# Optimization experiments

Measured on AMD Instinct MI355X. Metric: run time of the kernel, lower is better.

The kernel has to match this reference:

```python
import jax, jax.numpy as jnp
import numpy as np

N = 16384   # total gate nodes (64 graphs x 256 gates)
B = 64      # graphs in batch
E = 49152   # directed edges (avg in-degree 3)
Q = 32      # qubit_num
F = 256     # feat_dim
D = 2 * F   # node feature dim = 512
H = 2       # heads
A = 128     # action_num


def _gatv2(x, wl, wr, att, b, src, dst, n):
    # PyG GATv2Conv (concat=True, share_weights=False, negative_slope=0.2)
    h, c = att.shape
    xl = (x @ wl).reshape(n, h, c)   # source-side projection [N,H,C]
    xr = (x @ wr).reshape(n, h, c)   # target-side projection [N,H,C]
    e = jax.nn.leaky_relu(xl[src] + xr[dst], 0.2)       # [E,H,C]
    logit = jnp.einsum('ehc,hc->eh', e, att)             # [E,H]
    m = jax.ops.segment_max(logit, dst, num_segments=n)  # softmax over in-edges per target
    p = jnp.exp(logit - m[dst])
    den = jax.ops.segment_sum(p, dst, num_segments=n)
    alpha = p / den[dst]                                 # [E,H]
    out = jax.ops.segment_sum(alpha[:, :, None] * xl[src], dst, num_segments=n)
    return out.reshape(n, h * c) + b


def _forward(x, xt_w1, xt_b1, xt_w2, xt_b2,
             g0_wl, g0_wr, g0_att, g0_b,
             g1_wl, g1_wr, g1_att, g1_b,
             g2_wl, g2_wr, g2_att, g2_b,
             g3_wl, g3_wr, g3_att, g3_b,
             g4_wl, g4_wr, g4_att, g4_b,
             ln_w, ln_b, aggr_t,
             m_w1, m_b1, m_w2, m_b2, m_w3, m_b3,
             edge_index, batch):
    lr = lambda v: jax.nn.leaky_relu(v, 0.01)
    # x_trans: Linear -> LeakyReLU -> Linear, then fold qubit-pairs into one node
    h0 = lr(x @ xt_w1 + xt_b1) @ xt_w2 + xt_b2           # [2N, F]
    cx = h0.reshape(-1, D)                               # [N, 2F]
    n = cx.shape[0]
    # GATv2Conv default add_self_loops=True (inputs contain no self loops)
    sl = jnp.arange(n, dtype=edge_index.dtype)
    src = jnp.concatenate([edge_index[0], sl])
    dst = jnp.concatenate([edge_index[1], sl])
    res = cx
    h = lr(_gatv2(cx, g0_wl, g0_wr, g0_att, g0_b, src, dst, n))
    for wl_, wr_, att_, b_ in ((g1_wl, g1_wr, g1_att, g1_b),
                               (g2_wl, g2_wr, g2_att, g2_b),
                               (g3_wl, g3_wr, g3_att, g3_b)):
        h = lr(_gatv2(h, wl_, wr_, att_, b_, src, dst, n))
    h = lr(_gatv2(h, g4_wl, g4_wr, g4_att, g4_b, src, dst, n))
    h = h + res                                           # residual [N, 2F]
    # PyG LayerNorm(mode='graph'): normalize over nodes AND channels per graph
    cnt = jax.ops.segment_sum(jnp.ones((n,), h.dtype), batch, num_segments=B)
    norm = cnt * h.shape[1]
    mean = jax.ops.segment_sum(h.sum(-1), batch, num_segments=B) / norm
    hc = h - mean[batch][:, None]
    var = jax.ops.segment_sum((hc * hc).sum(-1), batch, num_segments=B) / norm
    h = hc / jnp.sqrt(var + 1e-5)[batch][:, None] * ln_w + ln_b
    # SoftmaxAggregation(learn=True): channel-wise softmax over nodes per graph
    logit = h * aggr_t
    mg = jax.ops.segment_max(logit, batch, num_segments=B)
    p = jnp.exp(logit - mg[batch])
    den = jax.ops.segment_sum(p, batch, num_segments=B)
    g = jax.ops.segment_sum((p / den[batch]) * h, batch, num_segments=B)  # [B, 2F]
    # head MLP 512->384->256->128
    o = lr(g @ m_w1 + m_b1)
    o = lr(o @ m_w2 + m_b2)
    return o @ m_w3 + m_b3


def setup_inputs() -> dict:
    key = jax.random.key(0)
    ks = iter(jax.random.split(key, 64))
    def rn(shp, s=0.05):
        return jax.random.normal(next(ks), shp, jnp.float32) * s
    d = {}
    d['x'] = jax.random.normal(next(ks), (2 * N, Q), jnp.float32)
    src = jax.random.randint(next(ks), (E,), 0, N, jnp.int32)
    off = jax.random.randint(next(ks), (E,), 1, N, jnp.int32)
    d['edge_index'] = jnp.stack([src, (src + off) % N])  # no self loops
    d['batch'] = jnp.arange(N, dtype=jnp.int32) // (N // B)
    d['xt_w1'] = rn((Q, F)); d['xt_b1'] = rn((F,))
    d['xt_w2'] = rn((F, F)); d['xt_b2'] = rn((F,))
    d['g0_wl'] = rn((D, H * D)); d['g0_wr'] = rn((D, H * D))
    d['g0_att'] = rn((H, D));    d['g0_b'] = rn((H * D,))
    for i in (1, 2, 3):
        d[f'g{i}_wl'] = rn((H * D, H * D)); d[f'g{i}_wr'] = rn((H * D, H * D))
        d[f'g{i}_att'] = rn((H, D));        d[f'g{i}_b'] = rn((H * D,))
    d['g4_wl'] = rn((H * D, D)); d['g4_wr'] = rn((H * D, D))
    d['g4_att'] = rn((1, D));    d['g4_b'] = rn((D,))
    d['ln_w'] = jnp.ones((D,), jnp.float32); d['ln_b'] = jnp.zeros((D,), jnp.float32)
    d['aggr_t'] = jnp.array(1.0, jnp.float32)
    d['m_w1'] = rn((D, 384)); d['m_b1'] = rn((384,))
    d['m_w2'] = rn((384, 256)); d['m_b2'] = rn((256,))
    d['m_w3'] = rn((256, A)); d['m_b3'] = rn((A,))
    return d


def reference(x, edge_index, batch, xt_w1, xt_b1, xt_w2, xt_b2,
              g0_wl, g0_wr, g0_att, g0_b,
              g1_wl, g1_wr, g1_att, g1_b,
              g2_wl, g2_wr, g2_att, g2_b,
              g3_wl, g3_wr, g3_att, g3_b,
              g4_wl, g4_wr, g4_att, g4_b,
              ln_w, ln_b, aggr_t,
              m_w1, m_b1, m_w2, m_b2, m_w3, m_b3):
    return _forward(x, xt_w1, xt_b1, xt_w2, xt_b2,
                    g0_wl, g0_wr, g0_att, g0_b,
                    g1_wl, g1_wr, g1_att, g1_b,
                    g2_wl, g2_wr, g2_att, g2_b,
                    g3_wl, g3_wr, g3_att, g3_b,
                    g4_wl, g4_wr, g4_att, g4_b,
                    ln_w, ln_b, aggr_t,
                    m_w1, m_b1, m_w2, m_b2, m_w3, m_b3,
                    edge_index, batch)
```

## Files before the change

### kernel.cpp

```cpp
#include <hip/hip_runtime.h>
#include <hip/hip_bf16.h>

typedef __hip_bfloat16 bf16;

#define NN 16384
#define BBG 64
#define EE 49152
#define ET (EE + NN)
#define DD 512
#define NG (NN / BBG)

__device__ __forceinline__ float b2f(bf16 v) { return __bfloat162float(v); }
__device__ __forceinline__ bf16 f2b(float v) { return __float2bfloat16(v); }
__device__ __forceinline__ float sb2f(short s) {
    unsigned u = ((unsigned)(unsigned short)s) << 16;
    return __builtin_bit_cast(float, u);
}
__device__ __forceinline__ short f2bs(float v) {
    bf16 b = f2b(v);
    return __builtin_bit_cast(short, b);
}
__device__ __forceinline__ int clampi(int v, int lo, int hi)
{
    return v < lo ? lo : (v > hi ? hi : v);
}

typedef __attribute__((ext_vector_type(8))) short bf16x8;
typedef __attribute__((ext_vector_type(4))) float f32x4;

#define AS1 __attribute__((address_space(1)))
#define AS3 __attribute__((address_space(3)))

__global__ __launch_bounds__(256) void gemm_mfma_bt(
    const bf16* __restrict__ A, const bf16* __restrict__ Bt,
    const float* __restrict__ bias, float* __restrict__ C,
    bf16* __restrict__ Cb, int M, int N, int K, float slope, int has_act)
{
    __shared__ bf16 As[128 * 32];
    __shared__ bf16 Bs[128 * 32];
    const int tid = threadIdx.x;
    const int w = tid >> 6;
    const int l = tid & 63;
    const int bm = blockIdx.y * 128;
    const int bn = blockIdx.x * 128;
    const int wrow = (w >> 1) * 64;
    const int wcol = (w & 1) * 64;
    const int quad = l >> 4;
    const int c16 = l & 15;

    const int lrow = l >> 2;
    const int lchunk = l & 3;
    const bf16* Ag = A + (size_t)(bm + w * 16 + lrow) * K + lchunk * 8;
    const bf16* Bg = Bt + (size_t)(bn + w * 16 + lrow) * K + lchunk * 8;
    char* AsB = (char*)As;
    char* BsB = (char*)Bs;

    f32x4 acc[4][4] = {};

    for (int k0 = 0; k0 < K; k0 += 32) {
        __builtin_amdgcn_global_load_lds((const AS1 void*)(Ag + k0),
            (AS3 void*)(AsB + w * 1024), 16, 0, 0);
        __builtin_amdgcn_global_load_lds((const AS1 void*)(Ag + (size_t)64 * K + k0),
            (AS3 void*)(AsB + 4096 + w * 1024), 16, 0, 0);
        __builtin_amdgcn_global_load_lds((const AS1 void*)(Bg + k0),
            (AS3 void*)(BsB + w * 1024), 16, 0, 0);
        __builtin_amdgcn_global_load_lds((const AS1 void*)(Bg + (size_t)64 * K + k0),
            (AS3 void*)(BsB + 4096 + w * 1024), 16, 0, 0);
        __syncthreads();

        bf16x8 a[4], b[4];
#pragma unroll
        for (int i = 0; i < 4; i++) {
            int ra = wrow + i * 16 + c16;
            a[i] = *(const bf16x8*)(AsB + ra * 64 + quad * 16);
            int rb = wcol + i * 16 + c16;
            b[i] = *(const bf16x8*)(BsB + rb * 64 + quad * 16);
        }
#pragma unroll
        for (int i = 0; i < 4; i++)
#pragma unroll
            for (int j = 0; j < 4; j++)
                acc[i][j] = __builtin_amdgcn_mfma_f32_16x16x32_bf16(
                    a[i], b[j], acc[i][j], 0, 0, 0);
        __syncthreads();
    }

#pragma unroll
    for (int i = 0; i < 4; i++) {
#pragma unroll
        for (int j = 0; j < 4; j++) {
            int col = bn + wcol + j * 16 + c16;
            float bv = bias ? bias[col] : 0.f;
#pragma unroll
            for (int r = 0; r < 4; r++) {
                int row = bm + wrow + i * 16 + quad * 4 + r;
                float v = acc[i][j][r] + bv;
                if (has_act) v = (v >= 0.f) ? v : v * slope;
                if (C)  C[(size_t)row * N + col] = v;
                if (Cb) Cb[(size_t)row * N + col] = f2b(v);
            }
        }
    }
}

__global__ __launch_bounds__(256) void gemm_mfma_dual(
    const bf16* __restrict__ A, const bf16* __restrict__ Bt,
    bf16* __restrict__ X0, bf16* __restrict__ X1,
    int M, int Ntot, int K, int HC)
{
    __shared__ bf16 As[128 * 32];
    __shared__ bf16 Bs[128 * 32];
    const int tid = threadIdx.x;
    const int w = tid >> 6;
    const int l = tid & 63;
    const int bm = blockIdx.y * 128;
    const int bn = blockIdx.x * 128;
    const int wrow = (w >> 1) * 64;
    const int wcol = (w & 1) * 64;
    const int quad = l >> 4;
    const int c16 = l & 15;

    const int lrow = l >> 2;
    const int lchunk = l & 3;
    const bf16* Ag = A + (size_t)(bm + w * 16 + lrow) * K + lchunk * 8;
    const bf16* Bg = Bt + (size_t)(bn + w * 16 + lrow) * K + lchunk * 8;
    char* AsB = (char*)As;
    char* BsB = (char*)Bs;

    f32x4 acc[4][4] = {};

    for (int k0 = 0; k0 < K; k0 += 32) {
        __builtin_amdgcn_global_load_lds((const AS1 void*)(Ag + k0),
            (AS3 void*)(AsB + w * 1024), 16, 0, 0);
        __builtin_amdgcn_global_load_lds((const AS1 void*)(Ag + (size_t)64 * K + k0),
            (AS3 void*)(AsB + 4096 + w * 1024), 16, 0, 0);
        __builtin_amdgcn_global_load_lds((const AS1 void*)(Bg + k0),
            (AS3 void*)(BsB + w * 1024), 16, 0, 0);
        __builtin_amdgcn_global_load_lds((const AS1 void*)(Bg + (size_t)64 * K + k0),
            (AS3 void*)(BsB + 4096 + w * 1024), 16, 0, 0);
        __syncthreads();

        bf16x8 a[4], b[4];
#pragma unroll
        for (int i = 0; i < 4; i++) {
            int ra = wrow + i * 16 + c16;
            a[i] = *(const bf16x8*)(AsB + ra * 64 + quad * 16);
            int rb = wcol + i * 16 + c16;
            b[i] = *(const bf16x8*)(BsB + rb * 64 + quad * 16);
        }
#pragma unroll
        for (int i = 0; i < 4; i++)
#pragma unroll
            for (int j = 0; j < 4; j++)
                acc[i][j] = __builtin_amdgcn_mfma_f32_16x16x32_bf16(
                    a[i], b[j], acc[i][j], 0, 0, 0);
        __syncthreads();
    }

#pragma unroll
    for (int i = 0; i < 4; i++) {
#pragma unroll
        for (int j = 0; j < 4; j++) {
            int col = bn + wcol + j * 16 + c16;
            bf16* dst = (col < HC) ? (X0 + col) : (X1 + col - HC);
#pragma unroll
            for (int r = 0; r < 4; r++) {
                int row = bm + wrow + i * 16 + quad * 4 + r;
                dst[(size_t)row * HC] = f2b(acc[i][j][r]);
            }
        }
    }
}

__global__ __launch_bounds__(256) void gemm_f32(
    const float* __restrict__ A, const float* __restrict__ W,
    const float* __restrict__ bias, float* __restrict__ C,
    int M, int N, int K, float slope, int has_act)
{
    const int BK = 16;
    __shared__ float Asm[BK][64 + 1];
    __shared__ float Wsm[BK][64 + 1];
    int tid = threadIdx.x;
    int bm = blockIdx.y * 64;
    int bn = blockIdx.x * 64;
    int tr = tid >> 4;
    int tc = tid & 15;
    float acc[4][4] = {};

    for (int k0 = 0; k0 < K; k0 += BK) {
        {
            int col = tid & 15;
            int row = tid >> 4;
#pragma unroll
            for (int p = 0; p < 4; p++) {
                int r = row + p * 16;
                Asm[col][r] = A[(size_t)(bm + r) * K + k0 + col];
            }
        }
        {
            int wc = tid & 63;
            int wr = tid >> 6;
#pragma unroll
            for (int p = 0; p < 4; p++) {
                int r = wr + p * 4;
                Wsm[r][wc] = W[(size_t)(k0 + r) * N + bn + wc];
            }
        }
        __syncthreads();
#pragma unroll
        for (int kk = 0; kk < BK; kk++) {
            float a[4], w[4];
#pragma unroll
            for (int i = 0; i < 4; i++) a[i] = Asm[kk][tr * 4 + i];
#pragma unroll
            for (int j = 0; j < 4; j++) w[j] = Wsm[kk][tc * 4 + j];
#pragma unroll
            for (int i = 0; i < 4; i++)
#pragma unroll
                for (int j = 0; j < 4; j++)
                    acc[i][j] += a[i] * w[j];
        }
        __syncthreads();
    }
#pragma unroll
    for (int i = 0; i < 4; i++) {
        int r = bm + tr * 4 + i;
#pragma unroll
        for (int j = 0; j < 4; j++) {
            int cn = bn + tc * 4 + j;
            float v = acc[i][j];
            if (bias) v += bias[cn];
            if (has_act) v = (v >= 0.f) ? v : v * slope;
            C[(size_t)r * N + cn] = v;
        }
    }
}

__global__ __launch_bounds__(256) void transpose_f2b2(
    const float* __restrict__ in0, bf16* __restrict__ out0,
    const float* __restrict__ in1, bf16* __restrict__ out1, int R, int C)
{
    const float* in = blockIdx.z ? in1 : in0;
    bf16* out = blockIdx.z ? out1 : out0;
    __shared__ float tile[32][33];
    int c0 = blockIdx.x * 32;
    int r0 = blockIdx.y * 32;
    int tx = threadIdx.x & 31;
    int ty = threadIdx.x >> 5;
#pragma unroll
    for (int k = 0; k < 4; k++) {
        int r = ty + k * 8;
        tile[r][tx] = in[(size_t)(r0 + r) * C + c0 + tx];
    }
    __syncthreads();
#pragma unroll
    for (int k = 0; k < 4; k++) {
        int rr = ty + k * 8;
        out[(size_t)(c0 + rr) * R + r0 + tx] = f2b(tile[tx][rr]);
    }
}

__global__ void f2b_vec(const float* __restrict__ in, bf16* __restrict__ out, int n)
{
    int i = blockIdx.x * 256 + threadIdx.x;
    if (i < n) out[i] = f2b(in[i]);
}

__global__ void count_deg(const int* __restrict__ ei, int* __restrict__ deg)
{
    int e = blockIdx.x * 256 + threadIdx.x;
    if (e >= ET) return;
    int d = (e < EE) ? ei[EE + e] : (e - EE);
    d = clampi(d, 0, NN - 1);
    atomicAdd(&deg[d], 1);
}

__global__ __launch_bounds__(256) void scan_deg(const int* __restrict__ deg,
                                                int* __restrict__ rs)
{
    __shared__ int part[256];
    __shared__ int psum[257];
    int tid = threadIdx.x;
    const int per = NN / 256;
    int base = tid * per;
    int s = 0;
    for (int i = 0; i < per; i++) s += deg[base + i];
    part[tid] = s;
    __syncthreads();
    if (tid == 0) {
        int acc = 0;
        for (int i = 0; i < 256; i++) { psum[i] = acc; acc += part[i]; }
        psum[256] = acc;
    }
    __syncthreads();
    int acc = psum[tid];
    for (int i = 0; i < per; i++) { rs[base + i] = acc; acc += deg[base + i]; }
    if (tid == 0) rs[NN] = psum[256];
}

__global__ void fill_csr(const int* __restrict__ ei, const int* __restrict__ rs,
                         int* __restrict__ cur, int* __restrict__ csrc)
{
    int e = blockIdx.x * 256 + threadIdx.x;
    if (e >= ET) return;
    int s, d;
    if (e < EE) { s = ei[e]; d = ei[EE + e]; } else { s = d = e - EE; }
    s = clampi(s, 0, NN - 1);
    d = clampi(d, 0, NN - 1);
    int pos = atomicAdd(&cur[d], 1);
    int slot = clampi(rs[d] + pos, 0, ET - 1);
    csrc[slot] = s;
}

template<int HC>
__global__ __launch_bounds__(256, 4) void gat_wave2(
    const bf16* __restrict__ xl, const bf16* __restrict__ xr,
    const float* __restrict__ att, const float* __restrict__ bias,
    const int* __restrict__ rs, const int* __restrict__ csrc,
    const float* __restrict__ res, float* __restrict__ out_f,
    bf16* __restrict__ out_b, float* __restrict__ lnsums)
{
    constexpr int CPL = HC / 64;
    constexpr int NV = CPL / 8;
    constexpr int PF = 6;
    const int tid = threadIdx.x;
    const int w = tid >> 6;
    const int lane = tid & 63;
    const int n = blockIdx.x * 4 + w;
    const int c0 = lane * CPL;

    int start = rs[n];
    int deg = clampi(rs[n + 1] - start, 1, 64);
    start = clampi(start, 0, ET - 1);
    int my_src = 0;
    if (lane < deg) my_src = clampi(csrc[start + lane], 0, NN - 1);

    float av[CPL], rv[CPL];
    {
        bf16x8 rp[NV];
#pragma unroll
        for (int v = 0; v < NV; v++)
            rp[v] = *(const bf16x8*)(xr + (size_t)n * HC + c0 + v * 8);
#pragma unroll
        for (int k = 0; k < CPL; k++) {
            rv[k] = sb2f(rp[k / 8][k % 8]);
            av[k] = att[c0 + k];
        }
    }

    bf16x8 rows[PF][NV];
#pragma unroll
    for (int r = 0; r < PF; r++) {
        if (r < deg) {
            int s = __shfl(my_src, r);
            const bf16* rp = xl + (size_t)s * HC + c0;
#pragma unroll
            for (int v = 0; v < NV; v++) rows[r][v] = *(const bf16x8*)(rp + v * 8);
        }
    }

    float m = -1e30f, den = 0.f;
    float acc[CPL];
#pragma unroll
    for (int k = 0; k < CPL; k++) acc[k] = 0.f;

    auto process = [&](bf16x8 (&rw)[NV]) {
        float part = 0.f;
#pragma unroll
        for (int k = 0; k < CPL; k++) {
            float x = sb2f(rw[k / 8][k % 8]);
            float u = x + rv[k];
            u = (u >= 0.f) ? u : 0.2f * u;
            part = fmaf(av[k], u, part);
        }
        if (HC == 1024) {
#pragma unroll
            for (int msk = 16; msk; msk >>= 1) part += __shfl_xor(part, msk);
        } else {
#pragma unroll
            for (int msk = 32; msk; msk >>= 1) part += __shfl_xor(part, msk);
        }
        float lg = part;
        float mn = fmaxf(m, lg);
        float r = __expf(m - mn);
        float pi = __expf(lg - mn);
        m = mn;
        den = den * r + pi;
#pragma unroll
        for (int k = 0; k < CPL; k++) {
            float x = sb2f(rw[k / 8][k % 8]);
            acc[k] = fmaf(acc[k], r, pi * x);
        }
    };

#pragma unroll
    for (int i = 0; i < PF; i++)
        if (i < deg) process(rows[i]);

    if (deg > PF) {
        bf16x8 curv[NV], nxt[NV];
        {
            int s = __shfl(my_src, PF);
            const bf16* rp = xl + (size_t)s * HC + c0;
#pragma unroll
            for (int v = 0; v < NV; v++) curv[v] = *(const bf16x8*)(rp + v * 8);
        }
        for (int i = PF; i < deg; i++) {
            if (i + 1 < deg) {
                int s = __shfl(my_src, i + 1);
                const bf16* rp = xl + (size_t)s * HC + c0;
#pragma unroll
                for (int v = 0; v < NV; v++) nxt[v] = *(const bf16x8*)(rp + v * 8);
            }
            process(curv);
#pragma unroll
            for (int v = 0; v < NV; v++) curv[v] = nxt[v];
        }
    }

    float inv = 1.f / den;
    float ls = 0.f, ls2 = 0.f;
    float vals[CPL];
#pragma unroll
    for (int k = 0; k < CPL; k++) {
        float v = fmaf(acc[k], inv, bias[c0 + k]);
        v = (v >= 0.f) ? v : 0.01f * v;
        vals[k] = v;
    }
    if (res) {
#pragma unroll
        for (int k = 0; k < CPL; k++) {
            vals[k] += res[(size_t)n * HC + c0 + k];
            ls += vals[k];
            ls2 += vals[k] * vals[k];
        }
#pragma unroll
        for (int v = 0; v < NV * 2; v++) {
            f32x4 ov;
#pragma unroll
            for (int k = 0; k < 4; k++) ov[k] = vals[v * 4 + k];
            *(f32x4*)(out_f + (size_t)n * HC + c0 + v * 4) = ov;
        }
    } else {
#pragma unroll
        for (int v = 0; v < NV; v++) {
            bf16x8 ov;
#pragma unroll
            for (int k = 0; k < 8; k++) ov[k] = f2bs(vals[v * 8 + k]);
            *(bf16x8*)(out_b + (size_t)n * HC + c0 + v * 8) = ov;
        }
    }

    if (lnsums) {
#pragma unroll
        for (int msk = 32; msk; msk >>= 1) {
            ls += __shfl_xor(ls, msk);
            ls2 += __shfl_xor(ls2, msk);
        }
        if (lane == 0) {
            int g = n >> 8;
            atomicAdd(&lnsums[g], ls);
            atomicAdd(&lnsums[BBG + g], ls2);
        }
    }
}

__global__ __launch_bounds__(256) void aggr_partial(
    const float* __restrict__ h, const float* __restrict__ lnsums,
    const float* __restrict__ lnw, const float* __restrict__ lnb,
    const float* __restrict__ t_, float* __restrict__ pm,
    float* __restrict__ pd, float* __restrict__ pa)
{
    int g = blockIdx.x, ch = blockIdx.y, nk = blockIdx.z;
    int tid = threadIdx.x;
    int c = ch * 256 + tid;
    const float tot = (float)(NG * DD);
    float S = lnsums[g], S2 = lnsums[BBG + g];
    float mu = S / tot;
    float iv = rsqrtf(fmaxf(S2 / tot - mu * mu, 0.f) + 1e-5f);
    float w = lnw[c], b = lnb[c], t = t_[0];
    size_t base = (size_t)g * NG * DD + (size_t)nk * 32 * DD + c;
    float m = -1e30f, den = 0.f, acc = 0.f;
    for (int i = 0; i < 32; i++) {
        float hn = (h[base + (size_t)i * DD] - mu) * iv * w + b;
        float lg = hn * t;
        if (lg > m) {
            float r = __expf(m - lg);
            den *= r; acc *= r; m = lg;
        }
        float p = __expf(lg - m);
        den += p; acc += p * hn;
    }
    size_t idx = (((size_t)g * 2 + ch) * 8 + nk) * 256 + tid;
    pm[idx] = m; pd[idx] = den; pa[idx] = acc;
}

__global__ __launch_bounds__(256) void aggr_combine(
    const float* __restrict__ pm, const float* __restrict__ pd,
    const float* __restrict__ pa, float* __restrict__ gout)
{
    int g = blockIdx.x, ch = blockIdx.y;
    int tid = threadIdx.x;
    size_t base = (((size_t)g * 2 + ch) * 8) * 256 + tid;
    float m = -1e30f;
#pragma unroll
    for (int k = 0; k < 8; k++) m = fmaxf(m, pm[base + k * 256]);
    float den = 0.f, acc = 0.f;
#pragma unroll
    for (int k = 0; k < 8; k++) {
        float r = __expf(pm[base + k * 256] - m);
        den += pd[base + k * 256] * r;
        acc += pa[base + k * 256] * r;
    }
    gout[(size_t)g * DD + ch * 256 + tid] = acc / den;
}

extern "C" void kernel_launch(void* const* d_in, const int* in_sizes, int n_in,
                              void* d_out, int out_size, void* d_ws, size_t ws_size,
                              hipStream_t stream)
{
    const float* x      = (const float*)d_in[0];
    const int*   ei     = (const int*)d_in[1];
    const float* xt_w1  = (const float*)d_in[3];
    const float* xt_b1  = (const float*)d_in[4];
    const float* xt_w2  = (const float*)d_in[5];
    const float* xt_b2  = (const float*)d_in[6];
    const float* ln_w   = (const float*)d_in[27];
    const float* ln_b   = (const float*)d_in[28];
    const float* aggr_t = (const float*)d_in[29];
    const float* m_w1   = (const float*)d_in[30];
    const float* m_b1   = (const float*)d_in[31];
    const float* m_w2   = (const float*)d_in[32];
    const float* m_b2   = (const float*)d_in[33];
    const float* m_w3   = (const float*)d_in[34];
    const float* m_b3   = (const float*)d_in[35];
    float* out = (float*)d_out;

    char* p = (char*)d_ws;
    auto take = [&](size_t bytes) {
        char* r = p;
        p += (bytes + 255) & ~(size_t)255;
        return r;
    };
    int* i_deg     = (int*)take((size_t)(NN + 1) * 4);
    int* i_rs      = (int*)take((size_t)(NN + 1) * 4);
    int* i_cur     = (int*)take((size_t)NN * 4);
    int* i_src     = (int*)take((size_t)ET * 4);
    float* f_sums  = (float*)take((size_t)2 * BBG * 4);
    float* f_pm    = (float*)take((size_t)BBG * 2 * 8 * 256 * 4);
    float* f_pd    = (float*)take((size_t)BBG * 2 * 8 * 256 * 4);
    float* f_pa    = (float*)take((size_t)BBG * 2 * 8 * 256 * 4);
    float* b_g     = (float*)take((size_t)BBG * DD * 4);
    float* b_m1    = (float*)take((size_t)BBG * 384 * 4);
    float* b_m2    = (float*)take((size_t)BBG * 256 * 4);
    float* b_res   = (float*)take((size_t)NN * DD * 4);
    float* b_h     = (float*)take((size_t)NN * DD * 4);
    bf16* b_resb   = (bf16*)take((size_t)NN * DD * 2);
    bf16* b_hb     = (bf16*)take((size_t)NN * 1024 * 2);
    bf16* b_xlb    = (bf16*)take((size_t)NN * 1024 * 2);
    bf16* b_xrb    = (bf16*)take((size_t)NN * 1024 * 2);
    bf16* b_xb     = (bf16*)take((size_t)2 * NN * 32 * 2);
    bf16* b_wcat   = (bf16*)take((size_t)2048 * 1024 * 2);
    bf16* b_w1b    = (bf16*)take((size_t)32 * 256 * 2);
    bf16* b_w2b    = (bf16*)take((size_t)256 * 256 * 2);
    bf16* b_t1b = b_hb;

    dim3 blk(256);

    hipMemsetAsync(i_deg, 0, (size_t)(NN + 1) * 4, stream);
    hipMemsetAsync(i_cur, 0, (size_t)NN * 4, stream);
    hipMemsetAsync(f_sums, 0, (size_t)2 * BBG * 4, stream);
    count_deg<<<ET / 256, blk, 0, stream>>>(ei, i_deg);
    scan_deg<<<1, blk, 0, stream>>>(i_deg, i_rs);
    fill_csr<<<ET / 256, blk, 0, stream>>>(ei, i_rs, i_cur, i_src);

    f2b_vec<<<(2 * NN * 32 + 255) / 256, blk, 0, stream>>>(x, b_xb, 2 * NN * 32);
    transpose_f2b2<<<dim3(256 / 32, 32 / 32, 1), blk, 0, stream>>>(
        xt_w1, b_w1b, xt_w1, b_w1b, 32, 256);
    transpose_f2b2<<<dim3(256 / 32, 256 / 32, 1), blk, 0, stream>>>(
        xt_w2, b_w2b, xt_w2, b_w2b, 256, 256);

    gemm_mfma_bt<<<dim3(256 / 128, 32768 / 128), blk, 0, stream>>>(
        b_xb, b_w1b, xt_b1, (float*)nullptr, b_t1b, 32768, 256, 32, 0.01f, 1);
    gemm_mfma_bt<<<dim3(256 / 128, 32768 / 128), blk, 0, stream>>>(
        b_t1b, b_w2b, xt_b2, b_res, b_resb, 32768, 256, 256, 0.f, 0);

    for (int L = 0; L < 5; L++) {
        const float* wl  = (const float*)d_in[7 + 4 * L];
        const float* wr  = (const float*)d_in[8 + 4 * L];
        const float* att = (const float*)d_in[9 + 4 * L];
        const float* gb  = (const float*)d_in[10 + 4 * L];
        int Fin = (L == 0) ? 512 : 1024;
        int HC  = (L == 4) ? 512 : 1024;
        const bf16* hin = (L == 0) ? b_resb : b_hb;

        transpose_f2b2<<<dim3(HC / 32, Fin / 32, 2), blk, 0, stream>>>(
            wl, b_wcat, wr, b_wcat + (size_t)HC * Fin, Fin, HC);
        gemm_mfma_dual<<<dim3(2 * HC / 128, NN / 128), blk, 0, stream>>>(
            hin, b_wcat, b_xlb, b_xrb, NN, 2 * HC, Fin, HC);
        if (L == 4) {
            gat_wave2<512><<<NN / 4, blk, 0, stream>>>(
                b_xlb, b_xrb, att, gb, i_rs, i_src,
                b_res, b_h, (bf16*)nullptr, f_sums);
        } else {
            gat_wave2<1024><<<NN / 4, blk, 0, stream>>>(
                b_xlb, b_xrb, att, gb, i_rs, i_src,
                (const float*)nullptr, (float*)nullptr, b_hb, (float*)nullptr);
        }
    }

    aggr_partial<<<dim3(BBG, 2, 8), blk, 0, stream>>>(
        b_h, f_sums, ln_w, ln_b, aggr_t, f_pm, f_pd, f_pa);
    aggr_combine<<<dim3(BBG, 2), blk, 0, stream>>>(f_pm, f_pd, f_pa, b_g);

    gemm_f32<<<dim3(384 / 64, 1), blk, 0, stream>>>(
        b_g, m_w1, m_b1, b_m1, 64, 384, 512, 0.01f, 1);
    gemm_f32<<<dim3(256 / 64, 1), blk, 0, stream>>>(
        b_m1, m_w2, m_b2, b_m2, 64, 256, 384, 0.01f, 1);
    gemm_f32<<<dim3(128 / 64, 1), blk, 0, stream>>>(
        b_m2, m_w3, m_b3, out, 64, 128, 256, 0.f, 0);
}
```

Baseline: 1.041 ms.

## Quantize GAT source features to FP8 and batch all weight transposes

For the first three GAT layers, the dual GEMM writes the source projection as FP8 e4m3 with a per-16-column bf16 scale, and a new gather kernel decodes these narrower rows to halve the random-gather bandwidth. All weight transposes are merged into one batched launch ahead of the layers. The residual and final-layer outputs move from fp32 to bf16. The gather prefetch is restructured into a rolling 3-deep pipeline. FP8 quantization of activations adds rounding error and extra shuffle and encode work in the GEMM epilogue.

```diff
diff --git a/kernel.cpp b/kernel.cpp
--- a/kernel.cpp
+++ b/kernel.cpp
@@ -25,6 +25,30 @@
     return v < lo ? lo : (v > hi ? hi : v);
 }
 
+__device__ __forceinline__ unsigned char enc_e4m3(float y)
+{
+    unsigned b = __builtin_bit_cast(unsigned, y);
+    unsigned s = (b >> 31) << 7;
+    float a = fabsf(y);
+    unsigned ab = b & 0x7fffffffu;
+    unsigned rb = ab + (1u << 19);
+    int e = (int)(rb >> 23) - 120;
+    unsigned m = (rb >> 20) & 7u;
+    unsigned qn = (unsigned)(e << 3) | m;
+    if (qn > 126u) qn = 126u;
+    unsigned qd = (unsigned)__float2int_rn(a * 512.f);
+    unsigned q = (a < 0.015625f) ? qd : qn;
+    return (unsigned char)(q | s);
+}
+__device__ __forceinline__ float dec_e4m3(unsigned q)
+{
+    unsigned e = (q >> 3) & 15u, m = q & 7u;
+    float nrm = __builtin_bit_cast(float, ((e + 120u) << 23) | (m << 20));
+    float dnm = (float)m * 0.001953125f;
+    float v = e ? nrm : dnm;
+    return (q & 128u) ? -v : v;
+}
+
 typedef __attribute__((ext_vector_type(8))) short bf16x8;
 typedef __attribute__((ext_vector_type(4))) float f32x4;
 
@@ -33,8 +57,8 @@
 
 __global__ __launch_bounds__(256) void gemm_mfma_bt(
     const bf16* __restrict__ A, const bf16* __restrict__ Bt,
-    const float* __restrict__ bias, float* __restrict__ C,
-    bf16* __restrict__ Cb, int M, int N, int K, float slope, int has_act)
+    const float* __restrict__ bias, bf16* __restrict__ Cb,
+    int M, int N, int K, float slope, int has_act)
 {
     __shared__ bf16 As[128 * 32];
     __shared__ bf16 Bs[128 * 32];
@@ -96,8 +120,7 @@
                 int row = bm + wrow + i * 16 + quad * 4 + r;
                 float v = acc[i][j][r] + bv;
                 if (has_act) v = (v >= 0.f) ? v : v * slope;
-                if (C)  C[(size_t)row * N + col] = v;
-                if (Cb) Cb[(size_t)row * N + col] = f2b(v);
+                Cb[(size_t)row * N + col] = f2b(v);
             }
         }
     }
@@ -105,8 +128,9 @@
 
 __global__ __launch_bounds__(256) void gemm_mfma_dual(
     const bf16* __restrict__ A, const bf16* __restrict__ Bt,
-    bf16* __restrict__ X0, bf16* __restrict__ X1,
-    int M, int Ntot, int K, int HC)
+    bf16* __restrict__ X0b, unsigned char* __restrict__ X0q,
+    bf16* __restrict__ X0s, bf16* __restrict__ X1,
+    int M, int K, int HC, int quant)
 {
     __shared__ bf16 As[128 * 32];
     __shared__ bf16 Bs[128 * 32];
@@ -162,11 +186,35 @@
 #pragma unroll
         for (int j = 0; j < 4; j++) {
             int col = bn + wcol + j * 16 + c16;
-            bf16* dst = (col < HC) ? (X0 + col) : (X1 + col - HC);
-#pragma unroll
-            for (int r = 0; r < 4; r++) {
-                int row = bm + wrow + i * 16 + quad * 4 + r;
-                dst[(size_t)row * HC] = f2b(acc[i][j][r]);
+            if (col < HC) {
+                if (quant) {
+#pragma unroll
+                    for (int r = 0; r < 4; r++) {
+                        int row = bm + wrow + i * 16 + quad * 4 + r;
+                        float v = acc[i][j][r];
+                        float mx = fabsf(v);
+#pragma unroll
+                        for (int msk = 8; msk; msk >>= 1)
+                            mx = fmaxf(mx, __shfl_xor(mx, msk));
+                        float sc = b2f(f2b(fmaxf(mx, 1e-20f) * (1.f / 448.f)));
+                        unsigned char q = enc_e4m3(v * (1.f / sc));
+                        X0q[(size_t)row * HC + col] = q;
+                        if (c16 == 0)
+                            X0s[(size_t)row * (HC / 16) + (col >> 4)] = f2b(sc);
+                    }
+                } else {
+#pragma unroll
+                    for (int r = 0; r < 4; r++) {
+                        int row = bm + wrow + i * 16 + quad * 4 + r;
+                        X0b[(size_t)row * HC + col] = f2b(acc[i][j][r]);
+                    }
+                }
+            } else {
+#pragma unroll
+                for (int r = 0; r < 4; r++) {
+                    int row = bm + wrow + i * 16 + quad * 4 + r;
+                    X1[(size_t)row * HC + col - HC] = f2b(acc[i][j][r]);
+                }
             }
         }
     }
@@ -236,15 +284,22 @@
     }
 }
 
-__global__ __launch_bounds__(256) void transpose_f2b2(
-    const float* __restrict__ in0, bf16* __restrict__ out0,
-    const float* __restrict__ in1, bf16* __restrict__ out1, int R, int C)
-{
-    const float* in = blockIdx.z ? in1 : in0;
-    bf16* out = blockIdx.z ? out1 : out0;
-    __shared__ float tile[32][33];
+struct TPackAll {
+    const float* in[12];
+    bf16* out[12];
+    int R[12], C[12];
+};
+
+__global__ __launch_bounds__(256) void transpose_batch(TPackAll pk)
+{
+    int z = blockIdx.z;
+    int R = pk.R[z], C = pk.C[z];
     int c0 = blockIdx.x * 32;
     int r0 = blockIdx.y * 32;
+    if (c0 >= C || r0 >= R) return;
+    const float* in = pk.in[z];
+    bf16* out = pk.out[z];
+    __shared__ float tile[32][33];
     int tx = threadIdx.x & 31;
     int ty = threadIdx.x >> 5;
 #pragma unroll
@@ -312,17 +367,13 @@
     csrc[slot] = s;
 }
 
-template<int HC>
-__global__ __launch_bounds__(256, 4) void gat_wave2(
-    const bf16* __restrict__ xl, const bf16* __restrict__ xr,
-    const float* __restrict__ att, const float* __restrict__ bias,
-    const int* __restrict__ rs, const int* __restrict__ csrc,
-    const float* __restrict__ res, float* __restrict__ out_f,
-    bf16* __restrict__ out_b, float* __restrict__ lnsums)
-{
-    constexpr int CPL = HC / 64;
-    constexpr int NV = CPL / 8;
-    constexpr int PF = 6;
+__global__ __launch_bounds__(256, 4) void gat_q(
+    const unsigned char* __restrict__ xlq, const bf16* __restrict__ xls,
+    const bf16* __restrict__ xr, const float* __restrict__ att,
+    const float* __restrict__ bias, const int* __restrict__ rs,
+    const int* __restrict__ csrc, bf16* __restrict__ out_b)
+{
+    constexpr int HC = 1024, CPL = 16;
     const int tid = threadIdx.x;
     const int w = tid >> 6;
     const int lane = tid & 63;
@@ -337,26 +388,12 @@
 
     float av[CPL], rv[CPL];
     {
-        bf16x8 rp[NV];
-#pragma unroll
-        for (int v = 0; v < NV; v++)
-            rp[v] = *(const bf16x8*)(xr + (size_t)n * HC + c0 + v * 8);
-#pragma unroll
-        for (int k = 0; k < CPL; k++) {
-            rv[k] = sb2f(rp[k / 8][k % 8]);
-            av[k] = att[c0 + k];
-        }
-    }
-
-    bf16x8 rows[PF][NV];
-#pragma unroll
-    for (int r = 0; r < PF; r++) {
-        if (r < deg) {
-            int s = __shfl(my_src, r);
-            const bf16* rp = xl + (size_t)s * HC + c0;
-#pragma unroll
-            for (int v = 0; v < NV; v++) rows[r][v] = *(const bf16x8*)(rp + v * 8);
-        }
+        bf16x8 r0 = *(const bf16x8*)(xr + (size_t)n * HC + c0);
+        bf16x8 r1 = *(const bf16x8*)(xr + (size_t)n * HC + c0 + 8);
+#pragma unroll
+        for (int k = 0; k < 8; k++) { rv[k] = sb2f(r0[k]); rv[8 + k] = sb2f(r1[k]); }
+#pragma unroll
+        for (int k = 0; k < CPL; k++) av[k] = att[c0 + k];
     }
 
     float m = -1e30f, den = 0.f;
@@ -364,22 +401,26 @@
 #pragma unroll
     for (int k = 0; k < CPL; k++) acc[k] = 0.f;
 
-    auto process = [&](bf16x8 (&rw)[NV]) {
+    auto loadrow = [&](int i, uint4& q, float& sc) {
+        int s = __shfl(my_src, i);
+        q = *(const uint4*)(xlq + (size_t)s * HC + c0);
+        sc = b2f(xls[(size_t)s * 64 + lane]);
+    };
+    auto process = [&](const uint4& q, float sc) {
+        float x[CPL];
+        const unsigned* qw = (const unsigned*)&q;
+#pragma unroll
+        for (int k = 0; k < CPL; k++)
+            x[k] = dec_e4m3((qw[k >> 2] >> ((k & 3) * 8)) & 255u) * sc;
         float part = 0.f;
 #pragma unroll
         for (int k = 0; k < CPL; k++) {
-            float x = sb2f(rw[k / 8][k % 8]);
-            float u = x + rv[k];
+            float u = x[k] + rv[k];
             u = (u >= 0.f) ? u : 0.2f * u;
             part = fmaf(av[k], u, part);
         }
-        if (HC == 1024) {
-#pragma unroll
-            for (int msk = 16; msk; msk >>= 1) part += __shfl_xor(part, msk);
-        } else {
-#pragma unroll
-            for (int msk = 32; msk; msk >>= 1) part += __shfl_xor(part, msk);
-        }
+#pragma unroll
+        for (int msk = 16; msk; msk >>= 1) part += __shfl_xor(part, msk);
         float lg = part;
         float mn = fmaxf(m, lg);
         float r = __expf(m - mn);
@@ -387,35 +428,119 @@
         m = mn;
         den = den * r + pi;
 #pragma unroll
+        for (int k = 0; k < CPL; k++) acc[k] = fmaf(acc[k], r, pi * x[k]);
+    };
+
+    uint4 cq, q1, q2, qn;
+    float cs, s1, s2, sn;
+    loadrow(0, cq, cs);
+    if (deg > 1) loadrow(1, q1, s1);
+    if (deg > 2) loadrow(2, q2, s2);
+    for (int i = 0; i < deg; i++) {
+        if (i + 3 < deg) loadrow(i + 3, qn, sn);
+        process(cq, cs);
+        cq = q1; cs = s1; q1 = q2; s1 = s2; q2 = qn; s2 = sn;
+    }
+
+    float inv = 1.f / den;
+    bf16x8 ov0, ov1;
+#pragma unroll
+    for (int k = 0; k < 8; k++) {
+        float v = fmaf(acc[k], inv, bias[c0 + k]);
+        v = (v >= 0.f) ? v : 0.01f * v;
+        ov0[k] = f2bs(v);
+        float v2 = fmaf(acc[8 + k], inv, bias[c0 + 8 + k]);
+        v2 = (v2 >= 0.f) ? v2 : 0.01f * v2;
+        ov1[k] = f2bs(v2);
+    }
+    *(bf16x8*)(out_b + (size_t)n * HC + c0) = ov0;
+    *(bf16x8*)(out_b + (size_t)n * HC + c0 + 8) = ov1;
+}
+
+template<int HC>
+__global__ __launch_bounds__(256) void gat_b(
+    const bf16* __restrict__ xl, const bf16* __restrict__ xr,
+    const float* __restrict__ att, const float* __restrict__ bias,
+    const int* __restrict__ rs, const int* __restrict__ csrc,
+    const bf16* __restrict__ res, bf16* __restrict__ out_b,
+    float* __restrict__ lnsums)
+{
+    constexpr int CPL = HC / 64;
+    constexpr int NV = CPL / 8;
+    const int tid = threadIdx.x;
+    const int w = tid >> 6;
+    const int lane = tid & 63;
+    const int n = blockIdx.x * 4 + w;
+    const int c0 = lane * CPL;
+
+    int start = rs[n];
+    int deg = clampi(rs[n + 1] - start, 1, 64);
+    start = clampi(start, 0, ET - 1);
+    int my_src = 0;
+    if (lane < deg) my_src = clampi(csrc[start + lane], 0, NN - 1);
+
+    float av[CPL], rv[CPL];
+    {
+        bf16x8 rp[NV];
+#pragma unroll
+        for (int v = 0; v < NV; v++)
+            rp[v] = *(const bf16x8*)(xr + (size_t)n * HC + c0 + v * 8);
+#pragma unroll
         for (int k = 0; k < CPL; k++) {
-            float x = sb2f(rw[k / 8][k % 8]);
+            rv[k] = sb2f(rp[k / 8][k % 8]);
+            av[k] = att[c0 + k];
+        }
+    }
+
+    float m = -1e30f, den = 0.f;
+    float acc[CPL];
+#pragma unroll
+    for (int k = 0; k < CPL; k++) acc[k] = 0.f;
+
+    auto loadrow = [&](int i, bf16x8* dst) {
+        int s = __shfl(my_src, i);
+        const bf16* rp = xl + (size_t)s * HC + c0;
+#pragma unroll
+        for (int v = 0; v < NV; v++) dst[v] = *(const bf16x8*)(rp + v * 8);
+    };
+
+    bf16x8 cur[NV], nx1[NV], nx2[NV];
+    loadrow(0, cur);
+    if (deg > 1) loadrow(1, nx1);
+    if (deg > 2) loadrow(2, nx2);
+
+    for (int i = 0; i < deg; i++) {
+        bf16x8 nxt[NV];
+        if (i + 3 < deg) loadrow(i + 3, nxt);
+
+        float part = 0.f;
+#pragma unroll
+        for (int k = 0; k < CPL; k++) {
+            float x = sb2f(cur[k / 8][k % 8]);
+            float u = x + rv[k];
+            u = (u >= 0.f) ? u : 0.2f * u;
+            part = fmaf(av[k], u, part);
+        }
+        if (HC == 1024) {
+#pragma unroll
+            for (int msk = 16; msk; msk >>= 1) part += __shfl_xor(part, msk);
+        } else {
+#pragma unroll
+            for (int msk = 32; msk; msk >>= 1) part += __shfl_xor(part, msk);
+        }
+        float lg = part;
+        float mn = fmaxf(m, lg);
+        float r = __expf(m - mn);
+        float pi = __expf(lg - mn);
+        m = mn;
+        den = den * r + pi;
+#pragma unroll
+        for (int k = 0; k < CPL; k++) {
+            float x = sb2f(cur[k / 8][k % 8]);
             acc[k] = fmaf(acc[k], r, pi * x);
         }
-    };
-
-#pragma unroll
-    for (int i = 0; i < PF; i++)
-        if (i < deg) process(rows[i]);
-
-    if (deg > PF) {
-        bf16x8 curv[NV], nxt[NV];
-        {
-            int s = __shfl(my_src, PF);
-            const bf16* rp = xl + (size_t)s * HC + c0;
-#pragma unroll
-            for (int v = 0; v < NV; v++) curv[v] = *(const bf16x8*)(rp + v * 8);
-        }
-        for (int i = PF; i < deg; i++) {
-            if (i + 1 < deg) {
-                int s = __shfl(my_src, i + 1);
-                const bf16* rp = xl + (size_t)s * HC + c0;
-#pragma unroll
-                for (int v = 0; v < NV; v++) nxt[v] = *(const bf16x8*)(rp + v * 8);
-            }
-            process(curv);
-#pragma unroll
-            for (int v = 0; v < NV; v++) curv[v] = nxt[v];
-        }
+#pragma unroll
+        for (int v = 0; v < NV; v++) { cur[v] = nx1[v]; nx1[v] = nx2[v]; nx2[v] = nxt[v]; }
     }
 
     float inv = 1.f / den;
@@ -428,27 +553,23 @@
         vals[k] = v;
     }
     if (res) {
+        bf16x8 rr[NV];
+#pragma unroll
+        for (int v = 0; v < NV; v++)
+            rr[v] = *(const bf16x8*)(res + (size_t)n * HC + c0 + v * 8);
 #pragma unroll
         for (int k = 0; k < CPL; k++) {
-            vals[k] += res[(size_t)n * HC + c0 + k];
+            vals[k] += sb2f(rr[k / 8][k % 8]);
             ls += vals[k];
             ls2 += vals[k] * vals[k];
         }
-#pragma unroll
-        for (int v = 0; v < NV * 2; v++) {
-            f32x4 ov;
-#pragma unroll
-            for (int k = 0; k < 4; k++) ov[k] = vals[v * 4 + k];
-            *(f32x4*)(out_f + (size_t)n * HC + c0 + v * 4) = ov;
-        }
-    } else {
-#pragma unroll
-        for (int v = 0; v < NV; v++) {
-            bf16x8 ov;
-#pragma unroll
-            for (int k = 0; k < 8; k++) ov[k] = f2bs(vals[v * 8 + k]);
-            *(bf16x8*)(out_b + (size_t)n * HC + c0 + v * 8) = ov;
-        }
+    }
+#pragma unroll
+    for (int v = 0; v < NV; v++) {
+        bf16x8 ov;
+#pragma unroll
+        for (int k = 0; k < 8; k++) ov[k] = f2bs(vals[v * 8 + k]);
+        *(bf16x8*)(out_b + (size_t)n * HC + c0 + v * 8) = ov;
     }
 
     if (lnsums) {
@@ -466,7 +587,7 @@
 }
 
 __global__ __launch_bounds__(256) void aggr_partial(
-    const float* __restrict__ h, const float* __restrict__ lnsums,
+    const bf16* __restrict__ h, const float* __restrict__ lnsums,
     const float* __restrict__ lnw, const float* __restrict__ lnb,
     const float* __restrict__ t_, float* __restrict__ pm,
     float* __restrict__ pd, float* __restrict__ pa)
@@ -482,7 +603,7 @@
     size_t base = (size_t)g * NG * DD + (size_t)nk * 32 * DD + c;
     float m = -1e30f, den = 0.f, acc = 0.f;
     for (int i = 0; i < 32; i++) {
-        float hn = (h[base + (size_t)i * DD] - mu) * iv * w + b;
+        float hn = (b2f(h[base + (size_t)i * DD]) - mu) * iv * w + b;
         float lg = hn * t;
         if (lg > m) {
             float r = __expf(m - lg);
@@ -553,17 +674,30 @@
     float* b_g     = (float*)take((size_t)BBG * DD * 4);
     float* b_m1    = (float*)take((size_t)BBG * 384 * 4);
     float* b_m2    = (float*)take((size_t)BBG * 256 * 4);
-    float* b_res   = (float*)take((size_t)NN * DD * 4);
-    float* b_h     = (float*)take((size_t)NN * DD * 4);
     bf16* b_resb   = (bf16*)take((size_t)NN * DD * 2);
+    bf16* b_h      = (bf16*)take((size_t)NN * DD * 2);
     bf16* b_hb     = (bf16*)take((size_t)NN * 1024 * 2);
     bf16* b_xlb    = (bf16*)take((size_t)NN * 1024 * 2);
     bf16* b_xrb    = (bf16*)take((size_t)NN * 1024 * 2);
+    unsigned char* b_xlq = (unsigned char*)take((size_t)NN * 1024);
+    bf16* b_xls    = (bf16*)take((size_t)NN * 64 * 2);
     bf16* b_xb     = (bf16*)take((size_t)2 * NN * 32 * 2);
-    bf16* b_wcat   = (bf16*)take((size_t)2048 * 1024 * 2);
+    bf16* b_wcat   = (bf16*)take((size_t)8 * 1024 * 1024 * 2);
     bf16* b_w1b    = (bf16*)take((size_t)32 * 256 * 2);
     bf16* b_w2b    = (bf16*)take((size_t)256 * 256 * 2);
     bf16* b_t1b = b_hb;
+
+    size_t woff[5], wlen[5];
+    {
+        size_t o = 0;
+        for (int L = 0; L < 5; L++) {
+            int Fin = (L == 0) ? 512 : 1024;
+            int HC  = (L == 4) ? 512 : 1024;
+            woff[L] = o;
+            wlen[L] = (size_t)2 * HC * Fin;
+            o += wlen[L];
+        }
+    }
 
     dim3 blk(256);
 
@@ -575,37 +709,51 @@
     fill_csr<<<ET / 256, blk, 0, stream>>>(ei, i_rs, i_cur, i_src);
 
     f2b_vec<<<(2 * NN * 32 + 255) / 256, blk, 0, stream>>>(x, b_xb, 2 * NN * 32);
-    transpose_f2b2<<<dim3(256 / 32, 32 / 32, 1), blk, 0, stream>>>(
-        xt_w1, b_w1b, xt_w1, b_w1b, 32, 256);
-    transpose_f2b2<<<dim3(256 / 32, 256 / 32, 1), blk, 0, stream>>>(
-        xt_w2, b_w2b, xt_w2, b_w2b, 256, 256);
+    {
+        TPackAll pk;
+        pk.in[0] = xt_w1; pk.out[0] = b_w1b; pk.R[0] = 32;  pk.C[0] = 256;
+        pk.in[1] = xt_w2; pk.out[1] = b_w2b; pk.R[1] = 256; pk.C[1] = 256;
+        for (int L = 0; L < 5; L++) {
+            int Fin = (L == 0) ? 512 : 1024;
+            int HC  = (L == 4) ? 512 : 1024;
+            pk.in[2 + 2 * L] = (const float*)d_in[7 + 4 * L];
+            pk.out[2 + 2 * L] = b_wcat + woff[L];
+            pk.R[2 + 2 * L] = Fin; pk.C[2 + 2 * L] = HC;
+            pk.in[3 + 2 * L] = (const float*)d_in[8 + 4 * L];
+            pk.out[3 + 2 * L] = b_wcat + woff[L] + (size_t)HC * Fin;
+            pk.R[3 + 2 * L] = Fin; pk.C[3 + 2 * L] = HC;
+        }
+        transpose_batch<<<dim3(32, 32, 12), blk, 0, stream>>>(pk);
+    }
 
     gemm_mfma_bt<<<dim3(256 / 128, 32768 / 128), blk, 0, stream>>>(
-        b_xb, b_w1b, xt_b1, (float*)nullptr, b_t1b, 32768, 256, 32, 0.01f, 1);
+        b_xb, b_w1b, xt_b1, b_t1b, 32768, 256, 32, 0.01f, 1);
     gemm_mfma_bt<<<dim3(256 / 128, 32768 / 128), blk, 0, stream>>>(
-        b_t1b, b_w2b, xt_b2, b_res, b_resb, 32768, 256, 256, 0.f, 0);
+        b_t1b, b_w2b, xt_b2, b_resb, 32768, 256, 256, 0.f, 0);
 
     for (int L = 0; L < 5; L++) {
-        const float* wl  = (const float*)d_in[7 + 4 * L];
-        const float* wr  = (const float*)d_in[8 + 4 * L];
         const float* att = (const float*)d_in[9 + 4 * L];
         const float* gb  = (const float*)d_in[10 + 4 * L];
         int Fin = (L == 0) ? 512 : 1024;
         int HC  = (L == 4) ? 512 : 1024;
+        int quant = (L <= 2) ? 1 : 0;
         const bf16* hin = (L == 0) ? b_resb : b_hb;
 
-        transpose_f2b2<<<dim3(HC / 32, Fin / 32, 2), blk, 0, stream>>>(
-            wl, b_wcat, wr, b_wcat + (size_t)HC * Fin, Fin, HC);
         gemm_mfma_dual<<<dim3(2 * HC / 128, NN / 128), blk, 0, stream>>>(
-            hin, b_wcat, b_xlb, b_xrb, NN, 2 * HC, Fin, HC);
-        if (L == 4) {
-            gat_wave2<512><<<NN / 4, blk, 0, stream>>>(
+            hin, b_wcat + woff[L],
+            quant ? (bf16*)nullptr : b_xlb, b_xlq, b_xls, b_xrb,
+            NN, Fin, HC, quant);
+        if (L <= 2) {
+            gat_q<<<NN / 4, blk, 0, stream>>>(
+                b_xlq, b_xls, b_xrb, att, gb, i_rs, i_src, b_hb);
+        } else if (L == 3) {
+            gat_b<1024><<<NN / 4, blk, 0, stream>>>(
                 b_xlb, b_xrb, att, gb, i_rs, i_src,
-                b_res, b_h, (bf16*)nullptr, f_sums);
+                (const bf16*)nullptr, b_hb, (float*)nullptr);
         } else {
-            gat_wave2<1024><<<NN / 4, blk, 0, stream>>>(
+            gat_b<512><<<NN / 4, blk, 0, stream>>>(
                 b_xlb, b_xrb, att, gb, i_rs, i_src,
-                (const float*)nullptr, (float*)nullptr, b_hb, (float*)nullptr);
+                b_resb, b_h, f_sums);
         }
     }
 
```

After: 1.163 ms. +11.7%, slower.
